# Kernel optimization log

Hardware: AMD Instinct MI355X
Metric: run time of the kernel (lower is better)

Reference implementation:

```python
import jax, jax.numpy as jnp
import numpy as np
import math

B, S, H = 8, 2048, 256

def setup_inputs() -> dict:
    key = jax.random.key(0)
    ks = jax.random.split(key, 7)
    stdv = 1.0 / math.sqrt(H)
    return {
        "k": jax.random.normal(ks[0], (B, S, H), dtype=jnp.float32),
        "q": jax.random.normal(ks[1], (B, S, H), dtype=jnp.float32),
        "v": jax.random.normal(ks[2], (B, S, H), dtype=jnp.float32),
        "mask": jax.random.bernoulli(ks[3], 0.5, (B, S, S)),  # bool, masked-out positions
        "W_query": jax.random.uniform(ks[4], (H, H), jnp.float32, -stdv, stdv),
        "W_key": jax.random.uniform(ks[5], (H, H), jnp.float32, -stdv, stdv),
        "W_val": jax.random.uniform(ks[6], (H, H), jnp.float32, -stdv, stdv),
    }

def reference(k, q, v, mask, W_query, W_key, W_val):
    Q = jnp.einsum("bsh,hd->bsd", q, W_query)
    K = jnp.einsum("bsh,hd->bsd", k, W_key)
    V = jnp.einsum("bsh,hd->bsd", v, W_val)
    norm = 1.0 / math.sqrt(Q.shape[-1])
    compat = norm * jnp.einsum("bqd,bkd->bqk", Q, K)  # [B,Sq,Sk]
    compat = jnp.where(mask, -jnp.inf, compat)
    score = jax.nn.softmax(compat, axis=-1)
    score = jnp.nan_to_num(score, nan=0.0)  # fully-masked rows -> all zeros
    return jnp.einsum("bqk,bkd->bqd", score, V)
```

## Files before the change

kernel.cpp:

```cpp
#include <hip/hip_runtime.h>


#define B_ 8
#define S_ 2048
#define H_ 256

typedef __attribute__((ext_vector_type(8))) short s16x8;
typedef __attribute__((ext_vector_type(4))) float f32x4;
typedef __attribute__((ext_vector_type(4))) unsigned short u16x4;
typedef __attribute__((ext_vector_type(8))) unsigned short u16x8;

#if __has_builtin(__builtin_amdgcn_exp2f)
#define EXP2F(x) __builtin_amdgcn_exp2f(x)
#else
#define EXP2F(x) exp2f(x)
#endif
#define L2E 1.4426950408889634f

__device__ __forceinline__ unsigned short f2bf(float f) {
  unsigned int u = __builtin_bit_cast(unsigned int, f);
  u += 0x7fffu + ((u >> 16) & 1u);
  return (unsigned short)(u >> 16);
}
__device__ __forceinline__ float bf2f(unsigned short h) {
  unsigned int u = ((unsigned int)h) << 16;
  return __builtin_bit_cast(float, u);
}
__device__ __forceinline__ f32x4 mfma_bf16(s16x8 a, s16x8 b, f32x4 c) {
  return __builtin_amdgcn_mfma_f32_16x16x32_bf16(a, b, c, 0, 0, 0);
}
__device__ __forceinline__ float sel4(const float v[4], int r) {
  float t0 = (r & 1) ? v[1] : v[0];
  float t1 = (r & 1) ? v[3] : v[2];
  return (r & 2) ? t1 : t0;
}
__device__ __forceinline__ void async16(const unsigned short* g, unsigned short* l) {
  __builtin_amdgcn_global_load_lds(
      (const __attribute__((address_space(1))) unsigned int*)g,
      (__attribute__((address_space(3))) unsigned int*)l, 16, 0, 0);
}

__global__ __launch_bounds__(256) void wt_kernel(
    const float* __restrict__ Wq, const float* __restrict__ Wk,
    const float* __restrict__ Wv, unsigned short* __restrict__ Wt) {
  __shared__ unsigned short tile[64 * 72];
  int z = blockIdx.x >> 4, x = blockIdx.x & 15;
  const float* W = (z == 0) ? Wq : (z == 1) ? Wk : Wv;
  int n0 = (x & 3) * 64, h0 = (x >> 2) * 64;
  int t = threadIdx.x;
#pragma unroll
  for (int j = 0; j < 4; ++j) {
    int c = j * 256 + t;
    int i = c >> 4, ch = c & 15;
    float4 f = *(const float4*)&W[(h0 + i) * 256 + n0 + ch * 4];
    u16x4 p;
    p[0] = f2bf(f.x); p[1] = f2bf(f.y); p[2] = f2bf(f.z); p[3] = f2bf(f.w);
    *(u16x4*)&tile[i * 72 + ch * 4] = p;
  }
  __syncthreads();
#pragma unroll
  for (int j = 0; j < 2; ++j) {
    int c = j * 256 + t;
    int nr = c >> 3, ch = c & 7;
    u16x8 o;
#pragma unroll
    for (int k = 0; k < 8; ++k) o[k] = tile[(ch * 8 + k) * 72 + nr];
    *(u16x8*)&Wt[z * 65536 + (n0 + nr) * 256 + h0 + ch * 8] = o;
  }
}

__global__ __launch_bounds__(256) void proj_kernel(
    const float* __restrict__ Xq, const float* __restrict__ Xk,
    const float* __restrict__ Xv, const unsigned short* __restrict__ Wt,
    unsigned short* __restrict__ Qb, unsigned short* __restrict__ Kb,
    unsigned short* __restrict__ Vt) {
  __shared__ unsigned short plds[16384];

  int z = blockIdx.x >> 8;
  int bx = blockIdx.x & 255;
  const float* X = (z == 0) ? Xq : (z == 1) ? Xk : Xv;
  const unsigned short* Wz = Wt + z * 65536;

  int t = threadIdx.x;
  int w = t >> 6, lane = t & 63, quad = lane >> 4, l15 = lane & 15;
  int m0 = bx * 64;
  const float* xrow = X + (size_t)(m0 + w * 16 + l15) * H_;

  f32x4 zero4 = {0.f, 0.f, 0.f, 0.f};
  f32x4 acc[16];
#pragma unroll
  for (int i = 0; i < 16; ++i) acc[i] = zero4;

#pragma unroll
  for (int j = 0; j < 4; ++j) {
    int c = j * 256 + t;
    int n = c >> 2, p = c & 3;
    async16(Wz + n * 256 + ((p ^ ((n >> 1) & 3)) << 3),
            plds + j * 2048 + w * 512);
  }
  float4 a0 = *(const float4*)(xrow + quad * 8);
  float4 a1 = *(const float4*)(xrow + quad * 8 + 4);

  for (int c8 = 0; c8 < 8; ++c8) {
    int cur = c8 & 1;
    unsigned short* Wc = plds + cur * 8192;
    __syncthreads();

    if (c8 < 7) {
      unsigned short* Wn = plds + (cur ^ 1) * 8192;
#pragma unroll
      for (int j = 0; j < 4; ++j) {
        int c = j * 256 + t;
        int n = c >> 2, p = c & 3;
        async16(Wz + n * 256 + (c8 + 1) * 32 + ((p ^ ((n >> 1) & 3)) << 3),
                Wn + j * 2048 + w * 512);
      }
    }
    float4 na0, na1;
    if (c8 < 7) {
      na0 = *(const float4*)(xrow + (c8 + 1) * 32 + quad * 8);
      na1 = *(const float4*)(xrow + (c8 + 1) * 32 + quad * 8 + 4);
    }
    s16x8 af;
    af[0] = (short)f2bf(a0.x); af[1] = (short)f2bf(a0.y);
    af[2] = (short)f2bf(a0.z); af[3] = (short)f2bf(a0.w);
    af[4] = (short)f2bf(a1.x); af[5] = (short)f2bf(a1.y);
    af[6] = (short)f2bf(a1.z); af[7] = (short)f2bf(a1.w);

#pragma unroll
    for (int nf = 0; nf < 16; ++nf) {
      int n = nf * 16 + l15;
      s16x8 bf = *(const s16x8*)&Wc[n * 32 + ((quad ^ ((n >> 1) & 3)) << 3)];
      acc[nf] = mfma_bf16(af, bf, acc[nf]);
    }
    a0 = na0; a1 = na1;
  }
  __syncthreads();

  float scale = (z == 0) ? 0.0625f : 1.0f;
  int b = m0 >> 11, s0 = m0 & 2047;
#pragma unroll
  for (int h = 0; h < 2; ++h) {
    if (h) __syncthreads();
    if (z < 2) {
#pragma unroll
      for (int nf2 = 0; nf2 < 8; ++nf2) {
        int n = nf2 * 16 + l15;
#pragma unroll
        for (int r = 0; r < 4; ++r)
          plds[(w * 16 + quad * 4 + r) * 136 + n] = f2bf(acc[h * 8 + nf2][r] * scale);
      }
      __syncthreads();
      unsigned short* Y = (z == 0) ? Qb : Kb;
#pragma unroll
      for (int j = 0; j < 4; ++j) {
        int c = j * 256 + t;
        int mr = c >> 4, ch = c & 15;
        u16x8 o = *(const u16x8*)&plds[mr * 136 + ch * 8];
        *(u16x8*)&Y[(size_t)(m0 + mr) * H_ + h * 128 + ch * 8] = o;
      }
    } else {
#pragma unroll
      for (int nf2 = 0; nf2 < 8; ++nf2) {
        int dl = nf2 * 16 + l15;
#pragma unroll
        for (int r = 0; r < 4; ++r)
          plds[dl * 72 + (w * 16 + quad * 4 + r)] = f2bf(acc[h * 8 + nf2][r]);
      }
      __syncthreads();
#pragma unroll
      for (int j = 0; j < 4; ++j) {
        int c = j * 256 + t;
        int dr = c >> 3, ch = c & 7;
        u16x8 o = *(const u16x8*)&plds[dr * 72 + ch * 8];
        *(u16x8*)&Vt[((size_t)b * H_ + h * 128 + dr) * S_ + s0 + ch * 8] = o;
      }
    }
  }
}

__global__ __launch_bounds__(256, 2) void attn_kernel(
    const unsigned short* __restrict__ Qb, const unsigned short* __restrict__ Kb,
    const unsigned short* __restrict__ Vt, const int* __restrict__ mask,
    unsigned short* __restrict__ Op, float* __restrict__ Ml,
    float* __restrict__ out) {
  __shared__ unsigned short lds[35328];
  unsigned short* Ps = lds + 32768;

  int t = threadIdx.x;
  int w = t >> 6, lane = t & 63, quad = lane >> 4, l15 = lane & 15;
  int b = blockIdx.x;
  int q0 = blockIdx.y * 64;
  int split = blockIdx.z, nsplit = gridDim.z;
  int kbeg = (64 * split) / nsplit, kend = (64 * (split + 1)) / nsplit;

  s16x8 qa[8];
  {
    const unsigned short* qp =
        Qb + ((size_t)b * S_ + q0 + w * 16 + l15) * H_ + quad * 8;
#pragma unroll
    for (int c = 0; c < 8; ++c) qa[c] = *(const s16x8*)(qp + 32 * c);
  }

  const unsigned short* Kbb = Kb + (size_t)b * S_ * H_;
  const unsigned short* Vbb = Vt + (size_t)b * H_ * S_;

  int krow = lane >> 5, kch = lane & 31;
  int vrow = lane >> 2, vch = lane & 3;

  f32x4 zero4 = {0.f, 0.f, 0.f, 0.f};
  f32x4 acc[16];
#pragma unroll
  for (int i = 0; i < 16; ++i) acc[i] = zero4;
  float l_r[4] = {0.f, 0.f, 0.f, 0.f};

  const int* mrowp[4];
#pragma unroll
  for (int r = 0; r < 4; ++r)
    mrowp[r] = mask + ((size_t)b * S_ + q0 + w * 16 + quad * 4 + r) * S_;

  {
    int k0 = kbeg * 32;
    unsigned short* Kd = lds;
    unsigned short* Vd = lds + 8192;
#pragma unroll
    for (int j = 0; j < 4; ++j) {
      int key = (w * 4 + j) * 2 + krow;
      async16(Kbb + ((size_t)(k0 + key) << 8) + ((kch ^ (key & 7)) << 3),
              Kd + (w * 4 + j) * 512);
      int d = w * 64 + j * 16 + vrow;
      async16(Vbb + ((size_t)d << 11) + k0 + ((vch ^ (d & 3)) << 3),
              Vd + (w * 64 + j * 16) * 32);
    }
  }
  int mw[2][4];
#pragma unroll
  for (int nf = 0; nf < 2; ++nf)
#pragma unroll
    for (int r = 0; r < 4; ++r)
      mw[nf][r] = mrowp[r][kbeg * 32 + nf * 16 + l15];

  for (int kt = kbeg; kt < kend; ++kt) {
    int cur = (kt - kbeg) & 1;
    unsigned short* Ksc = lds + cur * 16384;
    unsigned short* Vsc = Ksc + 8192;
    __syncthreads();

    if (kt + 1 < kend) {
      int k0 = (kt + 1) * 32;
      unsigned short* Kd = lds + (cur ^ 1) * 16384;
      unsigned short* Vd = Kd + 8192;
#pragma unroll
      for (int j = 0; j < 4; ++j) {
        int key = (w * 4 + j) * 2 + krow;
        async16(Kbb + ((size_t)(k0 + key) << 8) + ((kch ^ (key & 7)) << 3),
                Kd + (w * 4 + j) * 512);
        int d = w * 64 + j * 16 + vrow;
        async16(Vbb + ((size_t)d << 11) + k0 + ((vch ^ (d & 3)) << 3),
                Vd + (w * 64 + j * 16) * 32);
      }
    }
    int mwn[2][4];
    {
      int ktn = (kt + 1 < kend) ? kt + 1 : kt;
#pragma unroll
      for (int nf = 0; nf < 2; ++nf)
#pragma unroll
        for (int r = 0; r < 4; ++r)
          mwn[nf][r] = mrowp[r][ktn * 32 + nf * 16 + l15];
    }

    f32x4 sacc[2];
#pragma unroll
    for (int nf = 0; nf < 2; ++nf) sacc[nf] = zero4;
#pragma unroll
    for (int c = 0; c < 8; ++c) {
#pragma unroll
      for (int nf = 0; nf < 2; ++nf) {
        int n = nf * 16 + l15;
        s16x8 kb = *(const s16x8*)&Ksc[n * 256 + (((quad + 4 * c) ^ (n & 7)) << 3)];
        sacc[nf] = mfma_bf16(qa[c], kb, sacc[nf]);
      }
    }

    float pvv[2][4];
#pragma unroll
    for (int r = 0; r < 4; ++r) {
#pragma unroll
      for (int nf = 0; nf < 2; ++nf) {
        float p = mw[nf][r] ? 0.f : EXP2F(sacc[nf][r] * L2E);
        pvv[nf][r] = p;
        l_r[r] += p;
      }
    }

#pragma unroll
    for (int nf = 0; nf < 2; ++nf)
#pragma unroll
      for (int r = 0; r < 4; ++r) {
        int key = nf * 16 + l15;
        int ql = quad * 4 + r;
        Ps[w * 640 + ql * 40 + key] = f2bf(pvv[nf][r]);
      }

    {
      s16x8 bp = *(const s16x8*)&Ps[w * 640 + l15 * 40 + quad * 8];
#pragma unroll
      for (int mf = 0; mf < 16; ++mf) {
        int d = mf * 16 + l15;
        s16x8 av = *(const s16x8*)&Vsc[d * 32 + ((quad ^ (d & 3)) << 3)];
        acc[mf] = mfma_bf16(av, bp, acc[mf]);
      }
    }

#pragma unroll
    for (int nf = 0; nf < 2; ++nf)
#pragma unroll
      for (int r = 0; r < 4; ++r) mw[nf][r] = mwn[nf][r];
  }

#pragma unroll
  for (int r = 0; r < 4; ++r) {
#pragma unroll
    for (int d = 1; d < 16; d <<= 1) l_r[r] += __shfl_xor(l_r[r], d, 64);
  }

  if (gridDim.z == 1) {
    float l4[4];
    int srcl = (l15 >> 2) << 4;
#pragma unroll
    for (int r = 0; r < 4; ++r) l4[r] = __shfl(l_r[r], srcl, 64);
    float lq = sel4(l4, l15 & 3);
    float linv = (lq > 0.f) ? (1.0f / lq) : 0.f;
    float* op = out + ((size_t)b * S_ + q0 + w * 16 + l15) * H_ + quad * 4;
#pragma unroll
    for (int mf = 0; mf < 16; ++mf) {
      float4 o;
      o.x = acc[mf][0] * linv; o.y = acc[mf][1] * linv;
      o.z = acc[mf][2] * linv; o.w = acc[mf][3] * linv;
      *(float4*)(op + mf * 16) = o;
    }
  } else {
    int qg = q0 + w * 16 + l15;
    unsigned short* op =
        Op + (((size_t)split * B_ + b) * S_ + qg) * H_ + quad * 4;
#pragma unroll
    for (int mf = 0; mf < 16; ++mf) {
      u16x4 pk;
      pk[0] = f2bf(acc[mf][0]); pk[1] = f2bf(acc[mf][1]);
      pk[2] = f2bf(acc[mf][2]); pk[3] = f2bf(acc[mf][3]);
      *(u16x4*)(op + mf * 16) = pk;
    }
    if (l15 == 0) {
#pragma unroll
      for (int r = 0; r < 4; ++r) {
        int qr = q0 + w * 16 + quad * 4 + r;
        Ml[((size_t)split * B_ + b) * S_ + qr] = l_r[r];
      }
    }
  }
}

__global__ __launch_bounds__(1024) void combine_kernel(
    const unsigned short* __restrict__ Op, const float* __restrict__ Ml,
    float* __restrict__ out, int nsplit) {
  int q = blockIdx.x * 4 + (threadIdx.x >> 8);
  int b = blockIdx.y, d = threadIdx.x & 255;
  float osum = 0.f, lsum = 0.f;
  for (int i = 0; i < nsplit; ++i) {
    size_t ro = ((size_t)i * B_ + b) * S_ + q;
    lsum += Ml[ro];
    osum += bf2f(Op[ro * H_ + d]);
  }
  float linv = (lsum > 0.f) ? (1.0f / lsum) : 0.f;
  out[((size_t)b * S_ + q) * H_ + d] = osum * linv;
}

extern "C" void kernel_launch(void* const* d_in, const int* in_sizes, int n_in,
                              void* d_out, int out_size, void* d_ws, size_t ws_size,
                              hipStream_t stream) {
  const float* k_in = (const float*)d_in[0];
  const float* q_in = (const float*)d_in[1];
  const float* v_in = (const float*)d_in[2];
  const int* mask = (const int*)d_in[3];
  const float* Wq = (const float*)d_in[4];
  const float* Wk = (const float*)d_in[5];
  const float* Wv = (const float*)d_in[6];
  float* out = (float*)d_out;

  unsigned short* Qb = (unsigned short*)d_ws;
  unsigned short* Kb = Qb + (size_t)4194304;
  unsigned short* Vt = Kb + (size_t)4194304;
  unsigned short* Wt = Vt + (size_t)4194304;
  unsigned short* Op = Wt + (size_t)196608;
  float* Ml = (float*)(Op + (size_t)8388608);
  const size_t need = 42467328;
  int nsplit = (ws_size >= need) ? 2 : 1;

  hipLaunchKernelGGL(wt_kernel, dim3(48), dim3(256), 0, stream,
                     Wq, Wk, Wv, Wt);
  hipLaunchKernelGGL(proj_kernel, dim3(768), dim3(256), 0, stream,
                     q_in, k_in, v_in, Wt, Qb, Kb, Vt);
  hipLaunchKernelGGL(attn_kernel, dim3(8, 32, nsplit), dim3(256), 0, stream,
                     Qb, Kb, Vt, mask, Op, Ml, out);
  if (nsplit > 1)
    hipLaunchKernelGGL(combine_kernel, dim3(512, 8), dim3(1024), 0, stream,
                       Op, Ml, out, nsplit);
}
```

Baseline: 293.0 us.

## Double query rows per wave to reuse K/V tiles, add 4-way key split

Each wave now handles 32 query rows in two groups of 16 instead of 16, so every K and V fragment read from LDS feeds two MFMAs. This halves LDS/global K,V traffic per query. To keep the grid filled with half as many query blocks, the key dimension is split four ways when the workspace is large enough, with wave priority raised around the MFMA loops. In exchange, accumulator registers double, which may hurt occupancy or cause spills, and the combine step reads more partial outputs.

```diff
diff --git a/kernel.cpp b/kernel.cpp
--- a/kernel.cpp
+++ b/kernel.cpp
@@ -184,22 +184,23 @@
     const unsigned short* __restrict__ Vt, const int* __restrict__ mask,
     unsigned short* __restrict__ Op, float* __restrict__ Ml,
     float* __restrict__ out) {
-  __shared__ unsigned short lds[35328];
+  __shared__ unsigned short lds[37376];
   unsigned short* Ps = lds + 32768;
 
   int t = threadIdx.x;
   int w = t >> 6, lane = t & 63, quad = lane >> 4, l15 = lane & 15;
   int b = blockIdx.x;
-  int q0 = blockIdx.y * 64;
+  int q0 = blockIdx.y * 128;
   int split = blockIdx.z, nsplit = gridDim.z;
   int kbeg = (64 * split) / nsplit, kend = (64 * (split + 1)) / nsplit;
 
-  s16x8 qa[8];
-  {
+  s16x8 qa[2][8];
+#pragma unroll
+  for (int g = 0; g < 2; ++g) {
     const unsigned short* qp =
-        Qb + ((size_t)b * S_ + q0 + w * 16 + l15) * H_ + quad * 8;
-#pragma unroll
-    for (int c = 0; c < 8; ++c) qa[c] = *(const s16x8*)(qp + 32 * c);
+        Qb + ((size_t)b * S_ + q0 + w * 32 + g * 16 + l15) * H_ + quad * 8;
+#pragma unroll
+    for (int c = 0; c < 8; ++c) qa[g][c] = *(const s16x8*)(qp + 32 * c);
   }
 
   const unsigned short* Kbb = Kb + (size_t)b * S_ * H_;
@@ -209,15 +210,20 @@
   int vrow = lane >> 2, vch = lane & 3;
 
   f32x4 zero4 = {0.f, 0.f, 0.f, 0.f};
-  f32x4 acc[16];
-#pragma unroll
-  for (int i = 0; i < 16; ++i) acc[i] = zero4;
-  float l_r[4] = {0.f, 0.f, 0.f, 0.f};
-
-  const int* mrowp[4];
-#pragma unroll
-  for (int r = 0; r < 4; ++r)
-    mrowp[r] = mask + ((size_t)b * S_ + q0 + w * 16 + quad * 4 + r) * S_;
+  f32x4 acc[16][2];
+#pragma unroll
+  for (int i = 0; i < 16; ++i)
+#pragma unroll
+    for (int g = 0; g < 2; ++g) acc[i][g] = zero4;
+  float l_r[2][4] = {{0.f, 0.f, 0.f, 0.f}, {0.f, 0.f, 0.f, 0.f}};
+
+  const int* mrowp[2][4];
+#pragma unroll
+  for (int g = 0; g < 2; ++g)
+#pragma unroll
+    for (int r = 0; r < 4; ++r)
+      mrowp[g][r] =
+          mask + ((size_t)b * S_ + q0 + w * 32 + g * 16 + quad * 4 + r) * S_;
 
   {
     int k0 = kbeg * 32;
@@ -233,12 +239,14 @@
               Vd + (w * 64 + j * 16) * 32);
     }
   }
-  int mw[2][4];
-#pragma unroll
-  for (int nf = 0; nf < 2; ++nf)
-#pragma unroll
-    for (int r = 0; r < 4; ++r)
-      mw[nf][r] = mrowp[r][kbeg * 32 + nf * 16 + l15];
+  int mw[2][2][4];
+#pragma unroll
+  for (int g = 0; g < 2; ++g)
+#pragma unroll
+    for (int nf = 0; nf < 2; ++nf)
+#pragma unroll
+      for (int r = 0; r < 4; ++r)
+        mw[g][nf][r] = mrowp[g][r][kbeg * 32 + nf * 16 + l15];
 
   for (int kt = kbeg; kt < kend; ++kt) {
     int cur = (kt - kbeg) & 1;
@@ -260,103 +268,134 @@
                 Vd + (w * 64 + j * 16) * 32);
       }
     }
-    int mwn[2][4];
+    int mwn[2][2][4];
     {
       int ktn = (kt + 1 < kend) ? kt + 1 : kt;
 #pragma unroll
-      for (int nf = 0; nf < 2; ++nf)
-#pragma unroll
-        for (int r = 0; r < 4; ++r)
-          mwn[nf][r] = mrowp[r][ktn * 32 + nf * 16 + l15];
-    }
-
-    f32x4 sacc[2];
-#pragma unroll
-    for (int nf = 0; nf < 2; ++nf) sacc[nf] = zero4;
+      for (int g = 0; g < 2; ++g)
+#pragma unroll
+        for (int nf = 0; nf < 2; ++nf)
+#pragma unroll
+          for (int r = 0; r < 4; ++r)
+            mwn[g][nf][r] = mrowp[g][r][ktn * 32 + nf * 16 + l15];
+    }
+
+    f32x4 sacc[2][2];
+#pragma unroll
+    for (int g = 0; g < 2; ++g)
+#pragma unroll
+      for (int nf = 0; nf < 2; ++nf) sacc[g][nf] = zero4;
+    __builtin_amdgcn_s_setprio(1);
 #pragma unroll
     for (int c = 0; c < 8; ++c) {
 #pragma unroll
       for (int nf = 0; nf < 2; ++nf) {
         int n = nf * 16 + l15;
         s16x8 kb = *(const s16x8*)&Ksc[n * 256 + (((quad + 4 * c) ^ (n & 7)) << 3)];
-        sacc[nf] = mfma_bf16(qa[c], kb, sacc[nf]);
-      }
-    }
-
-    float pvv[2][4];
-#pragma unroll
-    for (int r = 0; r < 4; ++r) {
-#pragma unroll
-      for (int nf = 0; nf < 2; ++nf) {
-        float p = mw[nf][r] ? 0.f : EXP2F(sacc[nf][r] * L2E);
-        pvv[nf][r] = p;
-        l_r[r] += p;
-      }
-    }
-
-#pragma unroll
-    for (int nf = 0; nf < 2; ++nf)
-#pragma unroll
-      for (int r = 0; r < 4; ++r) {
-        int key = nf * 16 + l15;
-        int ql = quad * 4 + r;
-        Ps[w * 640 + ql * 40 + key] = f2bf(pvv[nf][r]);
-      }
+#pragma unroll
+        for (int g = 0; g < 2; ++g)
+          sacc[g][nf] = mfma_bf16(qa[g][c], kb, sacc[g][nf]);
+      }
+    }
+    __builtin_amdgcn_s_setprio(0);
+
+    float pvv[2][2][4];
+#pragma unroll
+    for (int g = 0; g < 2; ++g)
+#pragma unroll
+      for (int r = 0; r < 4; ++r)
+#pragma unroll
+        for (int nf = 0; nf < 2; ++nf) {
+          float p = mw[g][nf][r] ? 0.f : EXP2F(sacc[g][nf][r] * L2E);
+          pvv[g][nf][r] = p;
+          l_r[g][r] += p;
+        }
+
+#pragma unroll
+    for (int g = 0; g < 2; ++g)
+#pragma unroll
+      for (int nf = 0; nf < 2; ++nf)
+#pragma unroll
+        for (int r = 0; r < 4; ++r) {
+          int key = nf * 16 + l15;
+          int ql = g * 16 + quad * 4 + r;
+          Ps[w * 1152 + ql * 36 + key] = f2bf(pvv[g][nf][r]);
+        }
 
     {
-      s16x8 bp = *(const s16x8*)&Ps[w * 640 + l15 * 40 + quad * 8];
+      s16x8 bp[2];
+#pragma unroll
+      for (int g = 0; g < 2; ++g)
+        bp[g] = *(const s16x8*)&Ps[w * 1152 + (g * 16 + l15) * 36 + quad * 8];
+      __builtin_amdgcn_s_setprio(1);
 #pragma unroll
       for (int mf = 0; mf < 16; ++mf) {
         int d = mf * 16 + l15;
         s16x8 av = *(const s16x8*)&Vsc[d * 32 + ((quad ^ (d & 3)) << 3)];
-        acc[mf] = mfma_bf16(av, bp, acc[mf]);
-      }
-    }
-
-#pragma unroll
-    for (int nf = 0; nf < 2; ++nf)
-#pragma unroll
-      for (int r = 0; r < 4; ++r) mw[nf][r] = mwn[nf][r];
-  }
-
-#pragma unroll
-  for (int r = 0; r < 4; ++r) {
-#pragma unroll
-    for (int d = 1; d < 16; d <<= 1) l_r[r] += __shfl_xor(l_r[r], d, 64);
-  }
+#pragma unroll
+        for (int g = 0; g < 2; ++g)
+          acc[mf][g] = mfma_bf16(av, bp[g], acc[mf][g]);
+      }
+      __builtin_amdgcn_s_setprio(0);
+    }
+
+#pragma unroll
+    for (int g = 0; g < 2; ++g)
+#pragma unroll
+      for (int nf = 0; nf < 2; ++nf)
+#pragma unroll
+        for (int r = 0; r < 4; ++r) mw[g][nf][r] = mwn[g][nf][r];
+  }
+
+#pragma unroll
+  for (int g = 0; g < 2; ++g)
+#pragma unroll
+    for (int r = 0; r < 4; ++r) {
+#pragma unroll
+      for (int d = 1; d < 16; d <<= 1) l_r[g][r] += __shfl_xor(l_r[g][r], d, 64);
+    }
 
   if (gridDim.z == 1) {
-    float l4[4];
-    int srcl = (l15 >> 2) << 4;
-#pragma unroll
-    for (int r = 0; r < 4; ++r) l4[r] = __shfl(l_r[r], srcl, 64);
-    float lq = sel4(l4, l15 & 3);
-    float linv = (lq > 0.f) ? (1.0f / lq) : 0.f;
-    float* op = out + ((size_t)b * S_ + q0 + w * 16 + l15) * H_ + quad * 4;
-#pragma unroll
-    for (int mf = 0; mf < 16; ++mf) {
-      float4 o;
-      o.x = acc[mf][0] * linv; o.y = acc[mf][1] * linv;
-      o.z = acc[mf][2] * linv; o.w = acc[mf][3] * linv;
-      *(float4*)(op + mf * 16) = o;
+#pragma unroll
+    for (int g = 0; g < 2; ++g) {
+      float l4[4];
+      int srcl = (l15 >> 2) << 4;
+#pragma unroll
+      for (int r = 0; r < 4; ++r) l4[r] = __shfl(l_r[g][r], srcl, 64);
+      float lq = sel4(l4, l15 & 3);
+      float linv = (lq > 0.f) ? (1.0f / lq) : 0.f;
+      float* op =
+          out + ((size_t)b * S_ + q0 + w * 32 + g * 16 + l15) * H_ + quad * 4;
+#pragma unroll
+      for (int mf = 0; mf < 16; ++mf) {
+        float4 o;
+        o.x = acc[mf][g][0] * linv; o.y = acc[mf][g][1] * linv;
+        o.z = acc[mf][g][2] * linv; o.w = acc[mf][g][3] * linv;
+        *(float4*)(op + mf * 16) = o;
+      }
     }
   } else {
-    int qg = q0 + w * 16 + l15;
-    unsigned short* op =
-        Op + (((size_t)split * B_ + b) * S_ + qg) * H_ + quad * 4;
-#pragma unroll
-    for (int mf = 0; mf < 16; ++mf) {
-      u16x4 pk;
-      pk[0] = f2bf(acc[mf][0]); pk[1] = f2bf(acc[mf][1]);
-      pk[2] = f2bf(acc[mf][2]); pk[3] = f2bf(acc[mf][3]);
-      *(u16x4*)(op + mf * 16) = pk;
+#pragma unroll
+    for (int g = 0; g < 2; ++g) {
+      int qg = q0 + w * 32 + g * 16 + l15;
+      unsigned short* op =
+          Op + (((size_t)split * B_ + b) * S_ + qg) * H_ + quad * 4;
+#pragma unroll
+      for (int mf = 0; mf < 16; ++mf) {
+        u16x4 pk;
+        pk[0] = f2bf(acc[mf][g][0]); pk[1] = f2bf(acc[mf][g][1]);
+        pk[2] = f2bf(acc[mf][g][2]); pk[3] = f2bf(acc[mf][g][3]);
+        *(u16x4*)(op + mf * 16) = pk;
+      }
     }
     if (l15 == 0) {
 #pragma unroll
-      for (int r = 0; r < 4; ++r) {
-        int qr = q0 + w * 16 + quad * 4 + r;
-        Ml[((size_t)split * B_ + b) * S_ + qr] = l_r[r];
-      }
+      for (int g = 0; g < 2; ++g)
+#pragma unroll
+        for (int r = 0; r < 4; ++r) {
+          int qr = q0 + w * 32 + g * 16 + quad * 4 + r;
+          Ml[((size_t)split * B_ + b) * S_ + qr] = l_r[g][r];
+        }
     }
   }
 }
@@ -393,15 +432,18 @@
   unsigned short* Vt = Kb + (size_t)4194304;
   unsigned short* Wt = Vt + (size_t)4194304;
   unsigned short* Op = Wt + (size_t)196608;
-  float* Ml = (float*)(Op + (size_t)8388608);
-  const size_t need = 42467328;
-  int nsplit = (ws_size >= need) ? 2 : 1;
+  float* Ml = (float*)(Op + (size_t)16777216);
+  const size_t need4 = 59375616;
+  const size_t need2 = 42467328;
+  int nsplit = (ws_size >= need4) ? 4 : (ws_size >= need2) ? 2 : 1;
+  if (nsplit == 2) Ml = (float*)(Op + (size_t)8388608);
+  if (nsplit == 1) Ml = (float*)(Op);
 
   hipLaunchKernelGGL(wt_kernel, dim3(48), dim3(256), 0, stream,
                      Wq, Wk, Wv, Wt);
   hipLaunchKernelGGL(proj_kernel, dim3(768), dim3(256), 0, stream,
                      q_in, k_in, v_in, Wt, Qb, Kb, Vt);
-  hipLaunchKernelGGL(attn_kernel, dim3(8, 32, nsplit), dim3(256), 0, stream,
+  hipLaunchKernelGGL(attn_kernel, dim3(8, 16, nsplit), dim3(256), 0, stream,
                      Qb, Kb, Vt, mask, Op, Ml, out);
   if (nsplit > 1)
     hipLaunchKernelGGL(combine_kernel, dim3(512, 8), dim3(1024), 0, stream,
```

After: 437.5 us. 1.49x slower.

## Load K fragments directly from global into registers instead of LDS staging

Applied to the files above, without the earlier changes.

K tiles are no longer double-buffered through LDS. Each lane now loads its K fragments straight from global memory into registers at the start of each iteration, and only V stays staged in LDS. This roughly halves the LDS footprint, which may allow more resident blocks, and removes the LDS round trip for K. The change also raises wave priority around the MFMA sections and shrinks the P scratch stride. The cost is that the global K load latency is no longer hidden by prefetch, and each of the four waves redundantly loads the same K rows.

```diff
diff --git a/kernel.cpp b/kernel.cpp
--- a/kernel.cpp
+++ b/kernel.cpp
@@ -184,8 +184,8 @@
     const unsigned short* __restrict__ Vt, const int* __restrict__ mask,
     unsigned short* __restrict__ Op, float* __restrict__ Ml,
     float* __restrict__ out) {
-  __shared__ unsigned short lds[35328];
-  unsigned short* Ps = lds + 32768;
+  __shared__ unsigned short lds[18688];
+  unsigned short* Ps = lds + 16384;
 
   int t = threadIdx.x;
   int w = t >> 6, lane = t & 63, quad = lane >> 4, l15 = lane & 15;
@@ -205,7 +205,6 @@
   const unsigned short* Kbb = Kb + (size_t)b * S_ * H_;
   const unsigned short* Vbb = Vt + (size_t)b * H_ * S_;
 
-  int krow = lane >> 5, kch = lane & 31;
   int vrow = lane >> 2, vch = lane & 3;
 
   f32x4 zero4 = {0.f, 0.f, 0.f, 0.f};
@@ -214,20 +213,16 @@
   for (int i = 0; i < 16; ++i) acc[i] = zero4;
   float l_r[4] = {0.f, 0.f, 0.f, 0.f};
 
-  const int* mrowp[4];
+  const int* mrow[4];
 #pragma unroll
   for (int r = 0; r < 4; ++r)
-    mrowp[r] = mask + ((size_t)b * S_ + q0 + w * 16 + quad * 4 + r) * S_;
+    mrow[r] = mask + ((size_t)b * S_ + q0 + w * 16 + quad * 4 + r) * S_;
 
   {
     int k0 = kbeg * 32;
-    unsigned short* Kd = lds;
-    unsigned short* Vd = lds + 8192;
+    unsigned short* Vd = lds;
 #pragma unroll
     for (int j = 0; j < 4; ++j) {
-      int key = (w * 4 + j) * 2 + krow;
-      async16(Kbb + ((size_t)(k0 + key) << 8) + ((kch ^ (key & 7)) << 3),
-              Kd + (w * 4 + j) * 512);
       int d = w * 64 + j * 16 + vrow;
       async16(Vbb + ((size_t)d << 11) + k0 + ((vch ^ (d & 3)) << 3),
               Vd + (w * 64 + j * 16) * 32);
@@ -238,23 +233,30 @@
   for (int nf = 0; nf < 2; ++nf)
 #pragma unroll
     for (int r = 0; r < 4; ++r)
-      mw[nf][r] = mrowp[r][kbeg * 32 + nf * 16 + l15];
+      mw[nf][r] = mrow[r][kbeg * 32 + nf * 16 + l15];
 
   for (int kt = kbeg; kt < kend; ++kt) {
     int cur = (kt - kbeg) & 1;
-    unsigned short* Ksc = lds + cur * 16384;
-    unsigned short* Vsc = Ksc + 8192;
+    unsigned short* Vsc = lds + cur * 8192;
+
+    s16x8 kb0[8], kb1[8];
+    {
+      const unsigned short* kp0 =
+          Kbb + ((size_t)(kt * 32 + l15) << 8) + quad * 8;
+      const unsigned short* kp1 = kp0 + (16 << 8);
+#pragma unroll
+      for (int c = 0; c < 8; ++c) kb0[c] = *(const s16x8*)(kp0 + 32 * c);
+#pragma unroll
+      for (int c = 0; c < 8; ++c) kb1[c] = *(const s16x8*)(kp1 + 32 * c);
+    }
+
     __syncthreads();
 
     if (kt + 1 < kend) {
       int k0 = (kt + 1) * 32;
-      unsigned short* Kd = lds + (cur ^ 1) * 16384;
-      unsigned short* Vd = Kd + 8192;
+      unsigned short* Vd = lds + (cur ^ 1) * 8192;
 #pragma unroll
       for (int j = 0; j < 4; ++j) {
-        int key = (w * 4 + j) * 2 + krow;
-        async16(Kbb + ((size_t)(k0 + key) << 8) + ((kch ^ (key & 7)) << 3),
-                Kd + (w * 4 + j) * 512);
         int d = w * 64 + j * 16 + vrow;
         async16(Vbb + ((size_t)d << 11) + k0 + ((vch ^ (d & 3)) << 3),
                 Vd + (w * 64 + j * 16) * 32);
@@ -267,21 +269,18 @@
       for (int nf = 0; nf < 2; ++nf)
 #pragma unroll
         for (int r = 0; r < 4; ++r)
-          mwn[nf][r] = mrowp[r][ktn * 32 + nf * 16 + l15];
+          mwn[nf][r] = mrow[r][ktn * 32 + nf * 16 + l15];
     }
 
     f32x4 sacc[2];
-#pragma unroll
-    for (int nf = 0; nf < 2; ++nf) sacc[nf] = zero4;
+    sacc[0] = zero4; sacc[1] = zero4;
+    __builtin_amdgcn_s_setprio(1);
 #pragma unroll
     for (int c = 0; c < 8; ++c) {
-#pragma unroll
-      for (int nf = 0; nf < 2; ++nf) {
-        int n = nf * 16 + l15;
-        s16x8 kb = *(const s16x8*)&Ksc[n * 256 + (((quad + 4 * c) ^ (n & 7)) << 3)];
-        sacc[nf] = mfma_bf16(qa[c], kb, sacc[nf]);
-      }
-    }
+      sacc[0] = mfma_bf16(qa[c], kb0[c], sacc[0]);
+      sacc[1] = mfma_bf16(qa[c], kb1[c], sacc[1]);
+    }
+    __builtin_amdgcn_s_setprio(0);
 
     float pvv[2][4];
 #pragma unroll
@@ -300,17 +299,19 @@
       for (int r = 0; r < 4; ++r) {
         int key = nf * 16 + l15;
         int ql = quad * 4 + r;
-        Ps[w * 640 + ql * 40 + key] = f2bf(pvv[nf][r]);
+        Ps[w * 576 + ql * 36 + key] = f2bf(pvv[nf][r]);
       }
 
     {
-      s16x8 bp = *(const s16x8*)&Ps[w * 640 + l15 * 40 + quad * 8];
+      s16x8 bp = *(const s16x8*)&Ps[w * 576 + l15 * 36 + quad * 8];
+      __builtin_amdgcn_s_setprio(1);
 #pragma unroll
       for (int mf = 0; mf < 16; ++mf) {
         int d = mf * 16 + l15;
         s16x8 av = *(const s16x8*)&Vsc[d * 32 + ((quad ^ (d & 3)) << 3)];
         acc[mf] = mfma_bf16(av, bp, acc[mf]);
       }
+      __builtin_amdgcn_s_setprio(0);
     }
 
 #pragma unroll
```

New measurement: 381.9 us. +30.4%, slower.
